# Kernel optimization log

Hardware: AMD Instinct MI355X
Metric: run time of the kernel (lower is better)

Reference implementation:

```python
import jax, jax.numpy as jnp
import numpy as np

NUM_ROUTING = 3

def _squash(s):
    # squared_norm * s / ((1 + squared_norm) * sqrt(squared_norm)), norm over last dim
    sn = jnp.sum(s * s, axis=-1, keepdims=True)
    return sn * s / ((1.0 + sn) * jnp.sqrt(sn))

def setup_inputs() -> dict:
    key = jax.random.key(0)
    kx, kw = jax.random.split(key)
    B, IN_CAPS, IN_DIM, OUT_CAPS, OUT_DIM = 64, 8192, 8, 8, 16
    x = jax.random.normal(kx, (B, IN_CAPS, IN_DIM), dtype=jnp.float32)
    W = 0.01 * jax.random.normal(kw, (IN_CAPS, OUT_CAPS, IN_DIM, OUT_DIM), dtype=jnp.float32)
    return {"x": x, "W": W}

def reference(x, W):
    # x: [B, in_caps, in_dim]; W: [in_caps, out_caps, in_dim, out_dim]
    u_hat = jnp.einsum('ijnm,bin->bijm', W, x)          # [B, i, j, m]
    temp_u_hat = jax.lax.stop_gradient(u_hat)           # detach, routing uses no grads
    B, I, J = x.shape[0], W.shape[0], W.shape[1]
    b = jnp.zeros((B, I, J), dtype=x.dtype)
    for _ in range(NUM_ROUTING - 1):
        c = jax.nn.softmax(b, axis=2)                   # over out_caps j
        s = jnp.einsum('bij,bijm->bjm', c, temp_u_hat)  # [B, j, m]
        v = _squash(s)
        b = b + jnp.einsum('bjm,bijm->bij', v, temp_u_hat)  # agreement
    c = jax.nn.softmax(b, axis=2)
    s = jnp.einsum('bij,bijm->bjm', c, u_hat)
    return _squash(s)                                   # [B, out_caps, out_dim]
```

## Files before the change

kernel.cpp:

```cpp
#include <hip/hip_runtime.h>


#define BB      64
#define ICAPS   8192
#define NDIM    8
#define JCAPS   8
#define MDIM    16
#define NBLK    256
#define ICHUNK  (ICAPS / NBLK)
#define IG      8
#define NSTAGE  (ICHUNK / IG)
#define JW      4
#define MW      4
#define WJ_STRIDE (NDIM * MDIM + 4)
#define WI_STRIDE (JCAPS * WJ_STRIDE)
#define S_ELEMS  (BB * JCAPS * MDIM)

template <int MODE>
__global__ __launch_bounds__(512, 1) void caps_pass_kernel(
    const float* __restrict__ x, const float* __restrict__ W,
    const float* __restrict__ vsum, float* __restrict__ partial)
{
    __shared__ float Wlds[IG * WI_STRIDE];

    const int tid = threadIdx.x;
    const int b   = tid >> 3;
    const int g   = tid & 7;
    const int jh  = g >> 2;
    const int mq  = g & 3;
    const int blk = blockIdx.x;
    const int i0  = blk * ICHUNK;

    float s_acc[JW][MW];
    #pragma unroll
    for (int a = 0; a < JW; ++a)
        #pragma unroll
        for (int c = 0; c < MW; ++c) s_acc[a][c] = 0.f;

    float vreg[JW][MW];
    if (MODE == 1) {
        #pragma unroll
        for (int jj = 0; jj < JW; ++jj) {
            const float4 vv = *(const float4*)&vsum[(b * JCAPS + jh * JW + jj) * MDIM + mq * 4];
            vreg[jj][0] = vv.x; vreg[jj][1] = vv.y; vreg[jj][2] = vv.z; vreg[jj][3] = vv.w;
        }
    }

    for (int st = 0; st < NSTAGE; ++st) {
        {
            const int iL  = tid >> 6;
            const int rem = tid & 63;
            const int j   = rem >> 3;
            const int n   = rem & 7;
            const float4* src = (const float4*)(W + (size_t)(i0 + st * IG + iL) * 1024
                                                  + j * 128 + n * 16);
            float4* dst = (float4*)&Wlds[iL * WI_STRIDE + j * WJ_STRIDE + n * 16];
            dst[0] = src[0]; dst[1] = src[1]; dst[2] = src[2]; dst[3] = src[3];
        }
        __syncthreads();

        #pragma unroll
        for (int ii = 0; ii < IG; ++ii) {
            const int i = i0 + st * IG + ii;
            const float4 xa = *(const float4*)&x[((size_t)b * ICAPS + i) * NDIM];
            const float4 xb = *(const float4*)&x[((size_t)b * ICAPS + i) * NDIM + 4];
            const float xs[8] = {xa.x, xa.y, xa.z, xa.w, xb.x, xb.y, xb.z, xb.w};

            float u[JW][MW] = {};
            const float* wbase = &Wlds[ii * WI_STRIDE + (jh * JW) * WJ_STRIDE + mq * 4];
            #pragma unroll
            for (int jj = 0; jj < JW; ++jj) {
                #pragma unroll
                for (int n = 0; n < NDIM; ++n) {
                    const float4 wq = *(const float4*)&wbase[jj * WJ_STRIDE + n * MDIM];
                    u[jj][0] += xs[n] * wq.x;
                    u[jj][1] += xs[n] * wq.y;
                    u[jj][2] += xs[n] * wq.z;
                    u[jj][3] += xs[n] * wq.w;
                }
            }

            if (MODE == 0) {
                #pragma unroll
                for (int jj = 0; jj < JW; ++jj)
                    #pragma unroll
                    for (int mm = 0; mm < MW; ++mm) s_acc[jj][mm] += u[jj][mm];
            } else {
                float lp[JW];
                #pragma unroll
                for (int jj = 0; jj < JW; ++jj)
                    lp[jj] = u[jj][0] * vreg[jj][0] + u[jj][1] * vreg[jj][1]
                           + u[jj][2] * vreg[jj][2] + u[jj][3] * vreg[jj][3];
                #pragma unroll
                for (int jj = 0; jj < JW; ++jj) {
                    lp[jj] += __shfl_xor(lp[jj], 1);
                    lp[jj] += __shfl_xor(lp[jj], 2);
                }
                float lo[JW];
                #pragma unroll
                for (int jj = 0; jj < JW; ++jj) lo[jj] = __shfl_xor(lp[jj], 4);
                float mx = lp[0];
                #pragma unroll
                for (int jj = 1; jj < JW; ++jj) mx = fmaxf(mx, lp[jj]);
                #pragma unroll
                for (int jj = 0; jj < JW; ++jj) mx = fmaxf(mx, lo[jj]);
                float e[JW];
                float den = 0.f;
                #pragma unroll
                for (int jj = 0; jj < JW; ++jj) {
                    e[jj] = __expf(lp[jj] - mx);
                    den += e[jj];
                    den += __expf(lo[jj] - mx);
                }
                const float inv = 1.0f / den;
                #pragma unroll
                for (int jj = 0; jj < JW; ++jj) {
                    const float c = e[jj] * inv;
                    #pragma unroll
                    for (int mm = 0; mm < MW; ++mm) s_acc[jj][mm] += c * u[jj][mm];
                }
            }
        }
        __syncthreads();
    }

    const float sc = (MODE == 0) ? 0.125f : 1.0f;
    float* pp = partial + (size_t)blk * S_ELEMS + b * (JCAPS * MDIM);
    #pragma unroll
    for (int jj = 0; jj < JW; ++jj) {
        float4 o;
        o.x = s_acc[jj][0] * sc; o.y = s_acc[jj][1] * sc;
        o.z = s_acc[jj][2] * sc; o.w = s_acc[jj][3] * sc;
        *(float4*)&pp[(jh * JW + jj) * MDIM + mq * 4] = o;
    }
}

template <int FINAL>
__global__ __launch_bounds__(256) void caps_reduce_kernel(
    const float* __restrict__ partial, float* __restrict__ vsum, float* __restrict__ out)
{
    __shared__ float sd[256];
    const int bo  = blockIdx.x;
    const int tid = threadIdx.x;
    const int tl  = tid >> 3;
    const int kg  = tid & 7;
    const int t   = bo * 32 + tl;

    float ssum = 0.f;
    const float* p = partial + (size_t)kg * 32 * S_ELEMS + t;
    #pragma unroll
    for (int k = 0; k < 32; ++k) ssum += p[(size_t)k * S_ELEMS];
    sd[tid] = ssum;
    __syncthreads();

    if (tid < 32) {
        const int tt = bo * 32 + tid;
        float s = 0.f;
        #pragma unroll
        for (int q = 0; q < 8; ++q) s += sd[tid * 8 + q];
        float sn = s * s;
        sn += __shfl_xor(sn, 1);
        sn += __shfl_xor(sn, 2);
        sn += __shfl_xor(sn, 4);
        sn += __shfl_xor(sn, 8);
        const float v = s * sqrtf(sn) / (1.f + sn);
        if (FINAL) out[tt] = v;
        else       vsum[tt] += v;
    }
}

extern "C" void kernel_launch(void* const* d_in, const int* in_sizes, int n_in,
                              void* d_out, int out_size, void* d_ws, size_t ws_size,
                              hipStream_t stream)
{
    const float* x = (const float*)d_in[0];
    const float* W = (const float*)d_in[1];
    float* out = (float*)d_out;

    float* partial = (float*)d_ws;
    float* vsum    = partial + (size_t)NBLK * S_ELEMS;

    hipMemsetAsync(vsum, 0, S_ELEMS * sizeof(float), stream);

    caps_pass_kernel<0><<<NBLK, 512, 0, stream>>>(x, W, vsum, partial);
    caps_reduce_kernel<0><<<256, 256, 0, stream>>>(partial, vsum, nullptr);
    caps_pass_kernel<1><<<NBLK, 512, 0, stream>>>(x, W, vsum, partial);
    caps_reduce_kernel<0><<<256, 256, 0, stream>>>(partial, vsum, nullptr);
    caps_pass_kernel<1><<<NBLK, 512, 0, stream>>>(x, W, vsum, partial);
    caps_reduce_kernel<1><<<256, 256, 0, stream>>>(partial, vsum, out);
}
```

Baseline: 223.6 us.

## Drop LDS staging of W, remap threads to one out-capsule per lane

```diff
diff --git a/kernel.cpp b/kernel.cpp
--- a/kernel.cpp
+++ b/kernel.cpp
@@ -8,130 +8,90 @@
 #define MDIM    16
 #define NBLK    256
 #define ICHUNK  (ICAPS / NBLK)
-#define IG      8
-#define NSTAGE  (ICHUNK / IG)
-#define JW      4
-#define MW      4
-#define WJ_STRIDE (NDIM * MDIM + 4)
-#define WI_STRIDE (JCAPS * WJ_STRIDE)
-#define S_ELEMS  (BB * JCAPS * MDIM)
+#define S_ELEMS (BB * JCAPS * MDIM)
 
 template <int MODE>
-__global__ __launch_bounds__(512, 1) void caps_pass_kernel(
+__global__ __launch_bounds__(512, 2) void caps_pass_kernel(
     const float* __restrict__ x, const float* __restrict__ W,
     const float* __restrict__ vsum, float* __restrict__ partial)
 {
-    __shared__ float Wlds[IG * WI_STRIDE];
-
     const int tid = threadIdx.x;
     const int b   = tid >> 3;
-    const int g   = tid & 7;
-    const int jh  = g >> 2;
-    const int mq  = g & 3;
-    const int blk = blockIdx.x;
-    const int i0  = blk * ICHUNK;
+    const int j   = tid & 7;
+    const int i0  = blockIdx.x * ICHUNK;
 
-    float s_acc[JW][MW];
+    float s_acc[MDIM];
     #pragma unroll
-    for (int a = 0; a < JW; ++a)
-        #pragma unroll
-        for (int c = 0; c < MW; ++c) s_acc[a][c] = 0.f;
+    for (int m = 0; m < MDIM; ++m) s_acc[m] = 0.f;
 
-    float vreg[JW][MW];
+    float vreg[MDIM];
     if (MODE == 1) {
         #pragma unroll
-        for (int jj = 0; jj < JW; ++jj) {
-            const float4 vv = *(const float4*)&vsum[(b * JCAPS + jh * JW + jj) * MDIM + mq * 4];
-            vreg[jj][0] = vv.x; vreg[jj][1] = vv.y; vreg[jj][2] = vv.z; vreg[jj][3] = vv.w;
+        for (int mc = 0; mc < 4; ++mc) {
+            const float4 vv = *(const float4*)&vsum[(b * JCAPS + j) * MDIM + mc * 4];
+            vreg[mc * 4 + 0] = vv.x; vreg[mc * 4 + 1] = vv.y;
+            vreg[mc * 4 + 2] = vv.z; vreg[mc * 4 + 3] = vv.w;
         }
     }
 
-    for (int st = 0; st < NSTAGE; ++st) {
-        {
-            const int iL  = tid >> 6;
-            const int rem = tid & 63;
-            const int j   = rem >> 3;
-            const int n   = rem & 7;
-            const float4* src = (const float4*)(W + (size_t)(i0 + st * IG + iL) * 1024
-                                                  + j * 128 + n * 16);
-            float4* dst = (float4*)&Wlds[iL * WI_STRIDE + j * WJ_STRIDE + n * 16];
-            dst[0] = src[0]; dst[1] = src[1]; dst[2] = src[2]; dst[3] = src[3];
-        }
-        __syncthreads();
+    const float* xb = x + ((size_t)b * ICAPS + i0) * NDIM;
+    const float* Wj = W + (size_t)i0 * 1024 + j * 128;
+
+    #pragma unroll 2
+    for (int it = 0; it < ICHUNK; ++it) {
+        const float4 xa = *(const float4*)(xb + it * NDIM);
+        const float4 xc = *(const float4*)(xb + it * NDIM + 4);
+        const float xs[8] = {xa.x, xa.y, xa.z, xa.w, xc.x, xc.y, xc.z, xc.w};
+
+        const float* wrow = Wj + (size_t)it * 1024;
+
+        float u[MDIM];
+        #pragma unroll
+        for (int m = 0; m < MDIM; ++m) u[m] = 0.f;
 
         #pragma unroll
-        for (int ii = 0; ii < IG; ++ii) {
-            const int i = i0 + st * IG + ii;
-            const float4 xa = *(const float4*)&x[((size_t)b * ICAPS + i) * NDIM];
-            const float4 xb = *(const float4*)&x[((size_t)b * ICAPS + i) * NDIM + 4];
-            const float xs[8] = {xa.x, xa.y, xa.z, xa.w, xb.x, xb.y, xb.z, xb.w};
+        for (int n = 0; n < NDIM; ++n) {
+            const float4 w0 = *(const float4*)(wrow + n * MDIM);
+            const float4 w1 = *(const float4*)(wrow + n * MDIM + 4);
+            const float4 w2 = *(const float4*)(wrow + n * MDIM + 8);
+            const float4 w3 = *(const float4*)(wrow + n * MDIM + 12);
+            const float xn = xs[n];
+            u[0]  += xn * w0.x;  u[1]  += xn * w0.y;  u[2]  += xn * w0.z;  u[3]  += xn * w0.w;
+            u[4]  += xn * w1.x;  u[5]  += xn * w1.y;  u[6]  += xn * w1.z;  u[7]  += xn * w1.w;
+            u[8]  += xn * w2.x;  u[9]  += xn * w2.y;  u[10] += xn * w2.z;  u[11] += xn * w2.w;
+            u[12] += xn * w3.x;  u[13] += xn * w3.y;  u[14] += xn * w3.z;  u[15] += xn * w3.w;
+        }
 
-            float u[JW][MW] = {};
-            const float* wbase = &Wlds[ii * WI_STRIDE + (jh * JW) * WJ_STRIDE + mq * 4];
+        if (MODE == 0) {
             #pragma unroll
-            for (int jj = 0; jj < JW; ++jj) {
-                #pragma unroll
-                for (int n = 0; n < NDIM; ++n) {
-                    const float4 wq = *(const float4*)&wbase[jj * WJ_STRIDE + n * MDIM];
-                    u[jj][0] += xs[n] * wq.x;
-                    u[jj][1] += xs[n] * wq.y;
-                    u[jj][2] += xs[n] * wq.z;
-                    u[jj][3] += xs[n] * wq.w;
-                }
-            }
-
-            if (MODE == 0) {
-                #pragma unroll
-                for (int jj = 0; jj < JW; ++jj)
-                    #pragma unroll
-                    for (int mm = 0; mm < MW; ++mm) s_acc[jj][mm] += u[jj][mm];
-            } else {
-                float lp[JW];
-                #pragma unroll
-                for (int jj = 0; jj < JW; ++jj)
-                    lp[jj] = u[jj][0] * vreg[jj][0] + u[jj][1] * vreg[jj][1]
-                           + u[jj][2] * vreg[jj][2] + u[jj][3] * vreg[jj][3];
-                #pragma unroll
-                for (int jj = 0; jj < JW; ++jj) {
-                    lp[jj] += __shfl_xor(lp[jj], 1);
-                    lp[jj] += __shfl_xor(lp[jj], 2);
-                }
-                float lo[JW];
-                #pragma unroll
-                for (int jj = 0; jj < JW; ++jj) lo[jj] = __shfl_xor(lp[jj], 4);
-                float mx = lp[0];
-                #pragma unroll
-                for (int jj = 1; jj < JW; ++jj) mx = fmaxf(mx, lp[jj]);
-                #pragma unroll
-                for (int jj = 0; jj < JW; ++jj) mx = fmaxf(mx, lo[jj]);
-                float e[JW];
-                float den = 0.f;
-                #pragma unroll
-                for (int jj = 0; jj < JW; ++jj) {
-                    e[jj] = __expf(lp[jj] - mx);
-                    den += e[jj];
-                    den += __expf(lo[jj] - mx);
-                }
-                const float inv = 1.0f / den;
-                #pragma unroll
-                for (int jj = 0; jj < JW; ++jj) {
-                    const float c = e[jj] * inv;
-                    #pragma unroll
-                    for (int mm = 0; mm < MW; ++mm) s_acc[jj][mm] += c * u[jj][mm];
-                }
-            }
+            for (int m = 0; m < MDIM; ++m) s_acc[m] += u[m];
+        } else {
+            float lg = 0.f;
+            #pragma unroll
+            for (int m = 0; m < MDIM; ++m) lg += u[m] * vreg[m];
+            float mx = lg;
+            mx = fmaxf(mx, __shfl_xor(mx, 1));
+            mx = fmaxf(mx, __shfl_xor(mx, 2));
+            mx = fmaxf(mx, __shfl_xor(mx, 4));
+            const float e = __expf(lg - mx);
+            float den = e;
+            den += __shfl_xor(den, 1);
+            den += __shfl_xor(den, 2);
+            den += __shfl_xor(den, 4);
+            const float c = e / den;
+            #pragma unroll
+            for (int m = 0; m < MDIM; ++m) s_acc[m] += c * u[m];
         }
-        __syncthreads();
     }
 
     const float sc = (MODE == 0) ? 0.125f : 1.0f;
-    float* pp = partial + (size_t)blk * S_ELEMS + b * (JCAPS * MDIM);
+    float* pp = partial + (size_t)blockIdx.x * S_ELEMS + (b * JCAPS + j) * MDIM;
     #pragma unroll
-    for (int jj = 0; jj < JW; ++jj) {
+    for (int mc = 0; mc < 4; ++mc) {
         float4 o;
-        o.x = s_acc[jj][0] * sc; o.y = s_acc[jj][1] * sc;
-        o.z = s_acc[jj][2] * sc; o.w = s_acc[jj][3] * sc;
-        *(float4*)&pp[(jh * JW + jj) * MDIM + mq * 4] = o;
+        o.x = s_acc[mc * 4 + 0] * sc; o.y = s_acc[mc * 4 + 1] * sc;
+        o.z = s_acc[mc * 4 + 2] * sc; o.w = s_acc[mc * 4 + 3] * sc;
+        *(float4*)&pp[mc * 4] = o;
     }
 }
 
```

New measurement: 782.0 us. 250% more time.
